# Kernel optimization log

Measured on AMD Instinct MI355X. Metric: run time of the kernel, lower is better.

Reference implementation:

```python
import jax, jax.numpy as jnp
import numpy as np

N_HEAD = 16

def setup_inputs() -> dict:
    key = jax.random.key(0)
    k1, k2, k3 = jax.random.split(key, 3)
    B, T, E = 4, 2048, 1024
    x = jax.random.normal(k1, (B, T, E), dtype=jnp.float32)
    w_attn = jax.random.normal(k2, (4 * E, E), dtype=jnp.float32) * (1.0 / np.sqrt(E))
    b_attn = jax.random.normal(k3, (4 * E,), dtype=jnp.float32) * 0.02
    return {"x": x, "w_attn": w_attn, "b_attn": b_attn}

def reference(x, w_attn, b_attn):
    B, T, C = x.shape
    H = N_HEAD
    D = C // H  # head_dim
    qkv = x @ w_attn.T + b_attn                      # [B,T,4C]
    q, k, v = qkv[..., :C], qkv[..., C:2*C], qkv[..., 2*C:3*C]  # 4th chunk unused
    q = q.reshape(B, T, H, D).transpose(0, 2, 1, 3)  # [B,H,T,D]
    k = k.reshape(B, T, H, D).transpose(0, 2, 1, 3)
    v = v.reshape(B, T, H, D).transpose(0, 2, 1, 3)
    scale = 1.0 / np.sqrt(D)
    attn = jnp.einsum('bhqd,bhkd->bhqk', q, k) * scale  # [B,H,T,T]
    causal = jnp.tril(jnp.ones((T, T), dtype=bool))
    attn = jnp.where(causal[None, None], attn, -jnp.inf)
    attn = jax.nn.softmax(attn, axis=-1)
    y = jnp.einsum('bhqk,bhkd->bhqd', attn, v)       # [B,H,T,D]
    return y.transpose(0, 2, 1, 3).reshape(B, T, C)
```

## Files before the change

### kernel.cpp

```cpp
#include <hip/hip_runtime.h>
#include <math.h>


using short8 = __attribute__((ext_vector_type(8))) short;
using f32x4  = __attribute__((ext_vector_type(4))) float;

__device__ __forceinline__ ushort f2bf(float f) {
    union { float f; unsigned u; } x{f};
    unsigned r = x.u + 0x7fffu + ((x.u >> 16) & 1u);
    return (ushort)(r >> 16);
}
__device__ __forceinline__ ushort f2bf_ru(float f) {
    union { float f; unsigned u; } x{f};
    return (ushort)((x.u + 0x8000u) >> 16);
}

__device__ __forceinline__ void gload_lds16(const void* g, void* l) {
    __builtin_amdgcn_global_load_lds(
        (const __attribute__((address_space(1))) void*)g,
        (__attribute__((address_space(3))) void*)l, 16, 0, 0);
}

__global__ void cvt_f32_bf16(const float* __restrict__ src, ushort* __restrict__ dst, int n4) {
    int i = blockIdx.x * blockDim.x + threadIdx.x;
    if (i >= n4) return;
    float4 v = ((const float4*)src)[i];
    ushort4 o;
    o.x = f2bf(v.x); o.y = f2bf(v.y); o.z = f2bf(v.z); o.w = f2bf(v.w);
    ((ushort4*)dst)[i] = o;
}

__global__ __launch_bounds__(256) void qkv_gemm(
    const ushort* __restrict__ A, const ushort* __restrict__ W,
    const float* __restrict__ bias,
    ushort* __restrict__ Qo, ushort* __restrict__ Ko, ushort* __restrict__ Vt)
{
    __shared__ ushort As[128 * 64];
    __shared__ ushort Ws[128 * 64];
    const int bn = blockIdx.x, bm = blockIdx.y;
    const int tid = threadIdx.x;
    const int wave = tid >> 6, lane = tid & 63;
    const int quad = lane >> 4, l16 = lane & 15, l7 = l16 & 7;
    const int wm = (wave >> 1) * 64, wn = (wave & 1) * 64;

    const ushort* Abase = A + (size_t)(bm * 128) * 1024;
    const ushort* Wbase = W + (size_t)(bn * 128) * 1024;

    f32x4 acc[4][4];
#pragma unroll
    for (int i = 0; i < 4; i++)
#pragma unroll
        for (int j = 0; j < 4; j++) acc[i][j] = (f32x4){0.f, 0.f, 0.f, 0.f};

    for (int k0 = 0; k0 < 1024; k0 += 64) {
        __syncthreads();
#pragma unroll
        for (int j = 0; j < 4; j++) {
            const int rb = wave * 32 + j * 8;
            const int r  = rb + (lane >> 3);
            const int cc = (lane & 7) ^ (r & 7);
            gload_lds16(Abase + (size_t)r * 1024 + k0 + cc * 8, &As[rb * 64]);
            gload_lds16(Wbase + (size_t)r * 1024 + k0 + cc * 8, &Ws[rb * 64]);
        }
        __syncthreads();
        short8 af[4][2], wf[4][2];
#pragma unroll
        for (int t = 0; t < 4; t++)
#pragma unroll
            for (int kg = 0; kg < 2; kg++) {
                const int pc = ((kg * 4 + quad) ^ l7) * 8;
                af[t][kg] = *(const short8*)&As[(wm + t * 16 + l16) * 64 + pc];
                wf[t][kg] = *(const short8*)&Ws[(wn + t * 16 + l16) * 64 + pc];
            }
#pragma unroll
        for (int kg = 0; kg < 2; kg++)
#pragma unroll
            for (int tm = 0; tm < 4; tm++)
#pragma unroll
                for (int tn = 0; tn < 4; tn++)
                    acc[tm][tn] = __builtin_amdgcn_mfma_f32_16x16x32_bf16(af[tm][kg], wf[tn][kg], acc[tm][tn], 0, 0, 0);
    }

    const float SCALE_Q = 0.125f * 1.4426950408889634f;
#pragma unroll
    for (int tn = 0; tn < 4; tn++) {
        const int n = bn * 128 + wn + tn * 16 + l16;
        const float bv = bias[n];
#pragma unroll
        for (int tm = 0; tm < 4; tm++) {
            const int m0 = bm * 128 + wm + tm * 16 + quad * 4;
            const int b0 = m0 >> 11, t0 = m0 & 2047;
            if (n < 1024) {
                const int h = n >> 6, d = n & 63;
#pragma unroll
                for (int r = 0; r < 4; r++)
                    Qo[((size_t)(b0 * 16 + h) * 2048 + t0 + r) * 64 + d] = f2bf((acc[tm][tn][r] + bv) * SCALE_Q);
            } else if (n < 2048) {
                const int c = n - 1024, h = c >> 6, d = c & 63;
#pragma unroll
                for (int r = 0; r < 4; r++)
                    Ko[((size_t)(b0 * 16 + h) * 2048 + t0 + r) * 64 + d] = f2bf(acc[tm][tn][r] + bv);
            } else {
                const int c = n - 2048, h = c >> 6, d = c & 63;
                ushort4 pk;
                pk.x = f2bf(acc[tm][tn][0] + bv); pk.y = f2bf(acc[tm][tn][1] + bv);
                pk.z = f2bf(acc[tm][tn][2] + bv); pk.w = f2bf(acc[tm][tn][3] + bv);
                *(ushort4*)&Vt[((size_t)(b0 * 16 + h) * 64 + d) * 2048 + t0] = pk;
            }
        }
    }
}

__global__ __launch_bounds__(256) void attn_fwd(
    const ushort* __restrict__ Q, const ushort* __restrict__ K,
    const ushort* __restrict__ Vt, float* __restrict__ out)
{
    __shared__ ushort Ks[2][64 * 64];
    __shared__ ushort Vs[2][64 * 64];
    __shared__ ushort Ps[4][16 * 64];
    const int id = (int)blockIdx.x;
    const int c = id & 7, k = id >> 3;
    const int bh = c + 8 * (k & 7);
    const int qt = 15 - (k >> 3);
    const int b = bh >> 4, h = bh & 15;
    const int wave = threadIdx.x >> 6, lane = threadIdx.x & 63;
    const int quad = lane >> 4, l16 = lane & 15, l7 = l16 & 7;

    const ushort* Kbh = K  + (size_t)bh * 2048 * 64;
    const ushort* Vbh = Vt + (size_t)bh * 64 * 2048;
    ushort* Pw = Ps[wave];

    int qb[2];
    qb[0] = qt * 128 + wave * 16;
    qb[1] = qb[0] + 64;

    short8 qf[2][2];
#pragma unroll
    for (int qg = 0; qg < 2; qg++) {
        const ushort* Qp = Q + ((size_t)bh * 2048 + qb[qg] + l16) * 64;
        qf[qg][0] = *(const short8*)(Qp + quad * 8);
        qf[qg][1] = *(const short8*)(Qp + 32 + quad * 8);
    }

    f32x4 o[2][4];
#pragma unroll
    for (int qg = 0; qg < 2; qg++)
#pragma unroll
        for (int dg = 0; dg < 4; dg++) o[qg][dg] = (f32x4){0.f, 0.f, 0.f, 0.f};
    float lsum[2] = {0.f, 0.f};

    const int ntiles = 2 * qt + 2;

#define STAGE(k0_, bf_)                                                              \
    {                                                                                \
        _Pragma("unroll")                                                            \
        for (int j = 0; j < 2; j++) {                                                \
            const int rb = wave * 16 + j * 8;                                        \
            const int r  = rb + (lane >> 3);                                         \
            const int cc = (lane & 7) ^ (r & 7);                                     \
            gload_lds16(Kbh + (size_t)((k0_) + r) * 64 + cc * 8, &Ks[bf_][rb * 64]); \
            gload_lds16(Vbh + (size_t)r * 2048 + (k0_) + cc * 8, &Vs[bf_][rb * 64]); \
        }                                                                            \
    }

    STAGE(0, 0);
    int buf = 0, k0 = 0;
    for (int it = 0; it < ntiles; ++it, k0 += 64, buf ^= 1) {
        __syncthreads();
        if (it + 1 < ntiles) STAGE(k0 + 64, buf ^ 1);
        if (k0 > qb[1] + 15) continue;

        const bool act0 = k0 <= qb[0] + 15;

        short8 kf[4][2];
#pragma unroll
        for (int t = 0; t < 4; t++)
#pragma unroll
            for (int dh = 0; dh < 2; dh++)
                kf[t][dh] = *(const short8*)&Ks[buf][(t * 16 + l16) * 64 + (((dh * 4 + quad) ^ l7) * 8)];
        f32x4 s[2][4];
#pragma unroll
        for (int qg = 0; qg < 2; qg++) {
            if (qg == 0 && !act0) continue;
#pragma unroll
            for (int t = 0; t < 4; t++) {
                f32x4 z = (f32x4){0.f, 0.f, 0.f, 0.f};
                z = __builtin_amdgcn_mfma_f32_16x16x32_bf16(kf[t][0], qf[qg][0], z, 0, 0, 0);
                z = __builtin_amdgcn_mfma_f32_16x16x32_bf16(kf[t][1], qf[qg][1], z, 0, 0, 0);
                s[qg][t] = z;
            }
        }

        short8 vf[2][4];
#pragma unroll
        for (int kg = 0; kg < 2; kg++) {
            const int pc = ((kg * 4 + quad) ^ l7) * 8;
#pragma unroll
            for (int dg = 0; dg < 4; dg++)
                vf[kg][dg] = *(const short8*)&Vs[buf][(dg * 16 + l16) * 64 + pc];
        }

#pragma unroll
        for (int qg = 0; qg < 2; qg++) {
            if (qg == 0 && !act0) continue;
            const int q = qb[qg] + l16;
            float p[16], ps = 0.f;
            if (k0 + 63 > qb[qg]) {
#pragma unroll
                for (int t = 0; t < 4; t++)
#pragma unroll
                    for (int r = 0; r < 4; r++) {
                        const int key = k0 + t * 16 + quad * 4 + r;
                        const float sv = (key <= q) ? s[qg][t][r] : -INFINITY;
                        p[t * 4 + r] = __builtin_amdgcn_exp2f(sv);
                    }
            } else {
#pragma unroll
                for (int t = 0; t < 4; t++)
#pragma unroll
                    for (int r = 0; r < 4; r++)
                        p[t * 4 + r] = __builtin_amdgcn_exp2f(s[qg][t][r]);
            }
#pragma unroll
            for (int i = 0; i < 16; i++) ps += p[i];
            lsum[qg] += ps;
#pragma unroll
            for (int t = 0; t < 4; t++) {
                ushort4 pk;
                pk.x = f2bf_ru(p[t * 4 + 0]); pk.y = f2bf_ru(p[t * 4 + 1]);
                pk.z = f2bf_ru(p[t * 4 + 2]); pk.w = f2bf_ru(p[t * 4 + 3]);
                const int pc = ((2 * t + (quad >> 1)) ^ l7) * 8 + (quad & 1) * 4;
                *(ushort4*)(Pw + l16 * 64 + pc) = pk;
            }
#pragma unroll
            for (int kg = 0; kg < 2; kg++) {
                short8 pf = *(const short8*)(Pw + l16 * 64 + (((kg * 4 + quad) ^ l7) * 8));
#pragma unroll
                for (int dg = 0; dg < 4; dg++)
                    o[qg][dg] = __builtin_amdgcn_mfma_f32_16x16x32_bf16(vf[kg][dg], pf, o[qg][dg], 0, 0, 0);
            }
        }
    }
#undef STAGE

#pragma unroll
    for (int qg = 0; qg < 2; qg++) {
        float l = lsum[qg];
        l += __shfl_xor(l, 16);
        l += __shfl_xor(l, 32);
        const float rinv = 1.f / l;
        float* op = out + ((size_t)(b * 2048 + qb[qg] + l16)) * 1024 + h * 64;
#pragma unroll
        for (int dg = 0; dg < 4; dg++) {
            float4 v;
            v.x = o[qg][dg][0] * rinv; v.y = o[qg][dg][1] * rinv;
            v.z = o[qg][dg][2] * rinv; v.w = o[qg][dg][3] * rinv;
            *(float4*)(op + dg * 16 + quad * 4) = v;
        }
    }
}

extern "C" void kernel_launch(void* const* d_in, const int* in_sizes, int n_in,
                              void* d_out, int out_size, void* d_ws, size_t ws_size,
                              hipStream_t stream) {
    const float* x    = (const float*)d_in[0];
    const float* w    = (const float*)d_in[1];
    const float* bias = (const float*)d_in[2];

    ushort* xb  = (ushort*)d_ws;
    ushort* wb  = xb + 8388608;
    ushort* Qb  = wb + 3145728;
    ushort* Kb  = Qb + 8388608;
    ushort* Vtb = Kb + 8388608;

    cvt_f32_bf16<<<8192, 256, 0, stream>>>(x, xb, 2097152);
    cvt_f32_bf16<<<3072, 256, 0, stream>>>(w, wb, 786432);
    qkv_gemm<<<dim3(24, 64), 256, 0, stream>>>(xb, wb, bias, Qb, Kb, Vtb);
    attn_fwd<<<1024, 256, 0, stream>>>(Qb, Kb, Vtb, (float*)d_out);
}
```

Before: 223.5 us.

## Enlarge attention query tile to 256 rows and fuse fp32-to-bf16 conversion launches

Each attention block now processes four 64-row query groups (256 rows), so each staged K/V tile is reused across more queries, halving K/V global traffic per query. The grid is halved and launch bounds request two blocks per CU. The two input conversion kernels are merged into one launch, and bf16 packing uses a byte-permute instruction to build pairs. Risks include more register pressure, fewer blocks for load balancing under the causal mask, and V now using round-half-up instead of round-to-nearest-even.

```diff
diff --git a/kernel.cpp b/kernel.cpp
--- a/kernel.cpp
+++ b/kernel.cpp
@@ -10,9 +10,9 @@
     unsigned r = x.u + 0x7fffu + ((x.u >> 16) & 1u);
     return (ushort)(r >> 16);
 }
-__device__ __forceinline__ ushort f2bf_ru(float f) {
-    union { float f; unsigned u; } x{f};
-    return (ushort)((x.u + 0x8000u) >> 16);
+__device__ __forceinline__ unsigned pack_bf16_ru(float a, float b) {
+    union { float f; unsigned u; } x{a}, y{b};
+    return __builtin_amdgcn_perm(y.u + 0x8000u, x.u + 0x8000u, 0x07060302u);
 }
 
 __device__ __forceinline__ void gload_lds16(const void* g, void* l) {
@@ -21,13 +21,16 @@
         (__attribute__((address_space(3))) void*)l, 16, 0, 0);
 }
 
-__global__ void cvt_f32_bf16(const float* __restrict__ src, ushort* __restrict__ dst, int n4) {
+__global__ void cvt_all(const float* __restrict__ x, const float* __restrict__ w,
+                        ushort* __restrict__ xb, ushort* __restrict__ wb) {
     int i = blockIdx.x * blockDim.x + threadIdx.x;
-    if (i >= n4) return;
-    float4 v = ((const float4*)src)[i];
+    const float* src; ushort* dst; int j;
+    if (i < 2097152) { src = x; dst = xb; j = i; }
+    else             { src = w; dst = wb; j = i - 2097152; if (j >= 786432) return; }
+    float4 v = ((const float4*)src)[j];
     ushort4 o;
     o.x = f2bf(v.x); o.y = f2bf(v.y); o.z = f2bf(v.z); o.w = f2bf(v.w);
-    ((ushort4*)dst)[i] = o;
+    ((ushort4*)dst)[j] = o;
 }
 
 __global__ __launch_bounds__(256) void qkv_gemm(
@@ -102,16 +105,16 @@
                     Ko[((size_t)(b0 * 16 + h) * 2048 + t0 + r) * 64 + d] = f2bf(acc[tm][tn][r] + bv);
             } else {
                 const int c = n - 2048, h = c >> 6, d = c & 63;
-                ushort4 pk;
-                pk.x = f2bf(acc[tm][tn][0] + bv); pk.y = f2bf(acc[tm][tn][1] + bv);
-                pk.z = f2bf(acc[tm][tn][2] + bv); pk.w = f2bf(acc[tm][tn][3] + bv);
-                *(ushort4*)&Vt[((size_t)(b0 * 16 + h) * 64 + d) * 2048 + t0] = pk;
-            }
-        }
-    }
-}
-
-__global__ __launch_bounds__(256) void attn_fwd(
+                uint2 pk;
+                pk.x = pack_bf16_ru(acc[tm][tn][0] + bv, acc[tm][tn][1] + bv);
+                pk.y = pack_bf16_ru(acc[tm][tn][2] + bv, acc[tm][tn][3] + bv);
+                *(uint2*)&Vt[((size_t)(b0 * 16 + h) * 64 + d) * 2048 + t0] = pk;
+            }
+        }
+    }
+}
+
+__global__ __launch_bounds__(256, 2) void attn_fwd(
     const ushort* __restrict__ Q, const ushort* __restrict__ K,
     const ushort* __restrict__ Vt, float* __restrict__ out)
 {
@@ -119,9 +122,9 @@
     __shared__ ushort Vs[2][64 * 64];
     __shared__ ushort Ps[4][16 * 64];
     const int id = (int)blockIdx.x;
-    const int c = id & 7, k = id >> 3;
-    const int bh = c + 8 * (k & 7);
-    const int qt = 15 - (k >> 3);
+    const int x8 = id & 7, s = id >> 3;
+    const int bh = x8 + 8 * (s & 7);
+    const int qt = 7 - (s >> 3);
     const int b = bh >> 4, h = bh & 15;
     const int wave = threadIdx.x >> 6, lane = threadIdx.x & 63;
     const int quad = lane >> 4, l16 = lane & 15, l7 = l16 & 7;
@@ -130,26 +133,26 @@
     const ushort* Vbh = Vt + (size_t)bh * 64 * 2048;
     ushort* Pw = Ps[wave];
 
-    int qb[2];
-    qb[0] = qt * 128 + wave * 16;
-    qb[1] = qb[0] + 64;
-
-    short8 qf[2][2];
-#pragma unroll
-    for (int qg = 0; qg < 2; qg++) {
+    int qb[4];
+#pragma unroll
+    for (int j = 0; j < 4; j++) qb[j] = qt * 256 + wave * 16 + j * 64;
+
+    short8 qf[4][2];
+#pragma unroll
+    for (int qg = 0; qg < 4; qg++) {
         const ushort* Qp = Q + ((size_t)bh * 2048 + qb[qg] + l16) * 64;
         qf[qg][0] = *(const short8*)(Qp + quad * 8);
         qf[qg][1] = *(const short8*)(Qp + 32 + quad * 8);
     }
 
-    f32x4 o[2][4];
-#pragma unroll
-    for (int qg = 0; qg < 2; qg++)
+    f32x4 o[4][4];
+#pragma unroll
+    for (int qg = 0; qg < 4; qg++)
 #pragma unroll
         for (int dg = 0; dg < 4; dg++) o[qg][dg] = (f32x4){0.f, 0.f, 0.f, 0.f};
-    float lsum[2] = {0.f, 0.f};
-
-    const int ntiles = 2 * qt + 2;
+    float lsum[4] = {0.f, 0.f, 0.f, 0.f};
+
+    const int ntiles = 4 * qt + 4;
 
 #define STAGE(k0_, bf_)                                                              \
     {                                                                                \
@@ -168,9 +171,7 @@
     for (int it = 0; it < ntiles; ++it, k0 += 64, buf ^= 1) {
         __syncthreads();
         if (it + 1 < ntiles) STAGE(k0 + 64, buf ^ 1);
-        if (k0 > qb[1] + 15) continue;
-
-        const bool act0 = k0 <= qb[0] + 15;
+        if (k0 > qb[3] + 15) continue;
 
         short8 kf[4][2];
 #pragma unroll
@@ -178,31 +179,26 @@
 #pragma unroll
             for (int dh = 0; dh < 2; dh++)
                 kf[t][dh] = *(const short8*)&Ks[buf][(t * 16 + l16) * 64 + (((dh * 4 + quad) ^ l7) * 8)];
-        f32x4 s[2][4];
-#pragma unroll
-        for (int qg = 0; qg < 2; qg++) {
-            if (qg == 0 && !act0) continue;
+        short8 vf[2][4];
+#pragma unroll
+        for (int kg = 0; kg < 2; kg++) {
+            const int pc = ((kg * 4 + quad) ^ l7) * 8;
+#pragma unroll
+            for (int dg = 0; dg < 4; dg++)
+                vf[kg][dg] = *(const short8*)&Vs[buf][(dg * 16 + l16) * 64 + pc];
+        }
+
+#pragma unroll
+        for (int qg = 0; qg < 4; qg++) {
+            if (k0 > qb[qg] + 15) continue;
+            f32x4 sc[4];
 #pragma unroll
             for (int t = 0; t < 4; t++) {
                 f32x4 z = (f32x4){0.f, 0.f, 0.f, 0.f};
                 z = __builtin_amdgcn_mfma_f32_16x16x32_bf16(kf[t][0], qf[qg][0], z, 0, 0, 0);
                 z = __builtin_amdgcn_mfma_f32_16x16x32_bf16(kf[t][1], qf[qg][1], z, 0, 0, 0);
-                s[qg][t] = z;
-            }
-        }
-
-        short8 vf[2][4];
-#pragma unroll
-        for (int kg = 0; kg < 2; kg++) {
-            const int pc = ((kg * 4 + quad) ^ l7) * 8;
-#pragma unroll
-            for (int dg = 0; dg < 4; dg++)
-                vf[kg][dg] = *(const short8*)&Vs[buf][(dg * 16 + l16) * 64 + pc];
-        }
-
-#pragma unroll
-        for (int qg = 0; qg < 2; qg++) {
-            if (qg == 0 && !act0) continue;
+                sc[t] = z;
+            }
             const int q = qb[qg] + l16;
             float p[16], ps = 0.f;
             if (k0 + 63 > qb[qg]) {
@@ -211,7 +207,7 @@
 #pragma unroll
                     for (int r = 0; r < 4; r++) {
                         const int key = k0 + t * 16 + quad * 4 + r;
-                        const float sv = (key <= q) ? s[qg][t][r] : -INFINITY;
+                        const float sv = (key <= q) ? sc[t][r] : -INFINITY;
                         p[t * 4 + r] = __builtin_amdgcn_exp2f(sv);
                     }
             } else {
@@ -219,18 +215,18 @@
                 for (int t = 0; t < 4; t++)
 #pragma unroll
                     for (int r = 0; r < 4; r++)
-                        p[t * 4 + r] = __builtin_amdgcn_exp2f(s[qg][t][r]);
+                        p[t * 4 + r] = __builtin_amdgcn_exp2f(sc[t][r]);
             }
 #pragma unroll
             for (int i = 0; i < 16; i++) ps += p[i];
             lsum[qg] += ps;
 #pragma unroll
             for (int t = 0; t < 4; t++) {
-                ushort4 pk;
-                pk.x = f2bf_ru(p[t * 4 + 0]); pk.y = f2bf_ru(p[t * 4 + 1]);
-                pk.z = f2bf_ru(p[t * 4 + 2]); pk.w = f2bf_ru(p[t * 4 + 3]);
+                uint2 pk;
+                pk.x = pack_bf16_ru(p[t * 4 + 0], p[t * 4 + 1]);
+                pk.y = pack_bf16_ru(p[t * 4 + 2], p[t * 4 + 3]);
                 const int pc = ((2 * t + (quad >> 1)) ^ l7) * 8 + (quad & 1) * 4;
-                *(ushort4*)(Pw + l16 * 64 + pc) = pk;
+                *(uint2*)(Pw + l16 * 64 + pc) = pk;
             }
 #pragma unroll
             for (int kg = 0; kg < 2; kg++) {
@@ -244,7 +240,7 @@
 #undef STAGE
 
 #pragma unroll
-    for (int qg = 0; qg < 2; qg++) {
+    for (int qg = 0; qg < 4; qg++) {
         float l = lsum[qg];
         l += __shfl_xor(l, 16);
         l += __shfl_xor(l, 32);
@@ -273,8 +269,7 @@
     ushort* Kb  = Qb + 8388608;
     ushort* Vtb = Kb + 8388608;
 
-    cvt_f32_bf16<<<8192, 256, 0, stream>>>(x, xb, 2097152);
-    cvt_f32_bf16<<<3072, 256, 0, stream>>>(w, wb, 786432);
+    cvt_all<<<11264, 256, 0, stream>>>(x, w, xb, wb);
     qkv_gemm<<<dim3(24, 64), 256, 0, stream>>>(xb, wb, bias, Qb, Kb, Vtb);
-    attn_fwd<<<1024, 256, 0, stream>>>(Qb, Kb, Vtb, (float*)d_out);
-}
+    attn_fwd<<<512, 256, 0, stream>>>(Qb, Kb, Vtb, (float*)d_out);
+}
```

After: 227.6 us. No clear change (+1.9%).
